# Performance work log

Hardware: AMD Instinct MI355X
Metric: run time of the kernel (lower is better)

The kernel has to match this reference:

```python
import jax, jax.numpy as jnp
import numpy as np

B_, T_, F_, N_ = 16, 12, 32, 500
L_, K_ = 3, 2
DIL = (1, 2, 4)


def setup_inputs() -> dict:
    key = jax.random.key(0)
    ks = jax.random.split(key, 12)
    f = jnp.float32
    return {
        "node_embeddings": jax.random.normal(ks[0], (B_, T_, F_, N_), f),
        "B_mat": jax.random.normal(ks[1], (F_, F_), f) * 0.1,
        "static_MTE": jax.random.normal(ks[2], (T_, N_, N_), f),
        "learnable_adj": jax.random.normal(ks[3], (T_, N_, N_), f),
        "conv_w": jax.random.normal(ks[4], (L_, F_, F_, 1, K_), f) * 0.1,
        "conv_b": jnp.zeros((L_, F_), f),
        "gcn_w": jax.random.normal(ks[5], (L_, F_, F_), f) * 0.1,
        "gcn_b": jnp.zeros((L_, F_), f),
        "gate_w": jax.random.normal(ks[6], (F_, F_), f) * 0.1,
        "gate_b": jnp.zeros((F_,), f),
        "att_Wa": jax.random.normal(ks[7], (F_, F_), f) * 0.1,
        "att_ba": jnp.zeros((F_,), f),
        "att_v": jax.random.normal(ks[8], (F_, 1), f) * 0.1,
        "use_MTE": 1,
        "batch_index": 2,
        "is_training": 1,
    }


def reference(node_embeddings, B_mat, static_MTE, learnable_adj, conv_w, conv_b,
              gcn_w, gcn_b, gate_w, gate_b, att_Wa, att_ba, att_v,
              use_MTE, batch_index, is_training):
    Bz, T, Fd, N = node_embeddings.shape
    L = conv_w.shape[0]

    # ---- dynamic adjacency: relu->softmax of U_{t-k} B U_t^T, for every k ----
    U = jnp.transpose(node_embeddings, (0, 1, 3, 2))        # [B,T,N,F]
    U_t = U[:, -1]                                          # [B,N,F]
    scores = jnp.einsum('btnf,fg,bmg->btnm', U, B_mat, U_t)  # [B,T,N,N]
    dyn = jax.nn.softmax(jax.nn.relu(scores), axis=-1)
    # batch_index != 1, training: learnable adjacency accumulated with dynamic one
    batch_dyn = learnable_adj[None] + dyn                   # module state update; GCNConv
    del batch_dyn                                           # drops edge weights, so Y does not depend on it

    # ---- dilated layers ----
    # GCNConv over dense_to_sparse(softmax adjacency): all N*N entries > 0, edge
    # weights are discarded -> propagation matrix P = (J + I) / (N + 1)
    x = node_embeddings                                     # [B,T,F,N]
    res_agg = []
    for li in range(L):
        residual = x
        X = jnp.transpose(x, (0, 1, 3, 2))                  # [B,T,N,F]
        propX = (jnp.sum(X, axis=2, keepdims=True) + X) / (N + 1)
        gcn = jnp.einsum('btnf,fg->btng', propX, gcn_w[li]) + gcn_b[li]
        # use_gnn & use_MTE & use_dynamic_adj -> sigmoid gating (dropout = eval identity)
        gcn = jax.nn.sigmoid(jnp.einsum('btnf,fg->btng', gcn, gate_w) + gate_b)
        # causal-padded dilated temporal conv over T
        pad = (K_ - 1) * DIL[li]
        xp = jnp.pad(gcn, ((0, 0), (pad, 0), (0, 0), (0, 0)))   # [B,T+pad,N,F]
        xp = jnp.transpose(xp, (0, 3, 2, 1))                    # [B,F,N,T+pad]
        out = jax.lax.conv_general_dilated(
            xp, conv_w[li], window_strides=(1, 1), padding='VALID',
            rhs_dilation=(1, DIL[li]),
            dimension_numbers=('NCHW', 'OIHW', 'NCHW'))
        out = jax.nn.relu(out + conv_b[li][None, :, None, None])  # [B,F,N,T]
        res_agg.append(out[:, :, :, -1])                          # [B,F,N]
        x = jnp.transpose(out, (0, 3, 1, 2)) + residual           # [B,T,F,N]

    # ---- multi-range attention over layer outputs ----
    res = jnp.stack(res_agg, axis=3)                        # [B,F,N,L]
    res = jnp.transpose(res, (0, 2, 1, 3))                  # [B,N,F,L]
    xp2 = jnp.transpose(res, (0, 3, 1, 2))                  # [B,L,N,F]
    s = jnp.tanh(xp2 @ att_Wa + att_ba) @ att_v             # [B,L,N,1]
    # faithful to original: flat (B,L,N) buffer reinterpreted as (B,N,L)
    s = s.reshape(Bz, N, L)
    a = jax.nn.softmax(s, axis=2)                           # [B,N,L]
    Y = jnp.einsum('bnm,bnfm->bnf', a, res)                 # [B,N,F]
    return Y
```

## Files before the change

### kernel.cpp

```cpp
#include <hip/hip_runtime.h>
#include <math.h>

#define B_ 16
#define T_ 12
#define F_ 32
#define N_ 500
#define L_ 3
#define K_ 2
#define INV_N1 (1.0f / 501.0f)

__device__ __forceinline__ float sigmoidf_(float x) {
    return 1.f / (1.f + __expf(-x));
}

__global__ __launch_bounds__(256) void prep_kernel(
        const float* __restrict__ x0,
        const float* __restrict__ gcn_w, const float* __restrict__ gcn_b,
        const float* __restrict__ gate_w, const float* __restrict__ gate_b,
        float* __restrict__ Wc, float* __restrict__ bc,
        float* __restrict__ cs0, float* __restrict__ cs1,
        float* __restrict__ cs2) {
    const int bt = blockIdx.x;
    const int tid = threadIdx.x;

    if (tid < F_) {
        cs1[bt * F_ + tid] = 0.f;
        cs2[bt * F_ + tid] = 0.f;
    }

    const int f = tid >> 3, j = tid & 7;
    const float4* row = (const float4*)(x0 + ((size_t)bt * F_ + f) * N_);
    float s = 0.f;
    for (int j4 = j; j4 < 125; j4 += 8) {
        float4 v = row[j4];
        s += v.x + v.y + v.z + v.w;
    }
    s += __shfl_xor(s, 1, 64);
    s += __shfl_xor(s, 2, 64);
    s += __shfl_xor(s, 4, 64);
    if (j == 0) cs0[bt * F_ + f] = s;

    if (bt < L_) {
        const int li = bt;
        for (int idx = tid; idx < F_ * F_; idx += 256) {
            int fi = idx >> 5, fo = idx & 31;
            float a = 0.f;
#pragma unroll
            for (int m = 0; m < F_; ++m)
                a += gcn_w[(li * F_ + fi) * F_ + m] * gate_w[m * F_ + fo];
            Wc[li * F_ * F_ + idx] = a * INV_N1;
        }
        if (tid < F_) {
            float a = gate_b[tid];
#pragma unroll
            for (int m = 0; m < F_; ++m)
                a += gcn_b[li * F_ + m] * gate_w[m * F_ + tid];
            bc[li * F_ + tid] = a;
        }
    }
}

__global__ __launch_bounds__(512) void gcn_kernel(
        const float* __restrict__ xin,
        const float* __restrict__ Wc, const float* __restrict__ bc,
        const float* __restrict__ cs, int li, float* __restrict__ g) {
    __shared__ __align__(16) float sx[F_][128];
    __shared__ __align__(16) float sWc[F_ * F_];
    __shared__ float sbase[F_];

    const int blk = blockIdx.x;
    const int bt = blk >> 2, c = blk & 3;
    const int nbase = c * 128;
    const int nb4 = (c == 3) ? 29 : 32;
    const int tid = threadIdx.x;

    for (int idx = tid; idx < F_ * nb4; idx += 512) {
        int f = idx / nb4, j4 = idx % nb4;
        float4 v = *(const float4*)(xin + ((size_t)bt * F_ + f) * N_ + nbase + 4 * j4);
        ((float4*)&sx[f][0])[j4] = v;
    }
    for (int idx = tid; idx < 256; idx += 512)
        ((float4*)sWc)[idx] = ((const float4*)(Wc + li * F_ * F_))[idx];
    if (tid < F_) {
        float a = bc[li * F_ + tid];
#pragma unroll
        for (int fi = 0; fi < F_; ++fi)
            a += cs[bt * F_ + fi] * Wc[li * F_ * F_ + fi * F_ + tid];
        sbase[tid] = a;
    }
    __syncthreads();

    const int n = tid & 127, q = tid >> 7;
    const int gn = nbase + n;
    if (gn < N_) {
        float acc[8];
#pragma unroll
        for (int jj = 0; jj < 8; ++jj) acc[jj] = sbase[q * 8 + jj];
#pragma unroll
        for (int fi = 0; fi < F_; ++fi) {
            float xv = sx[fi][n];
#pragma unroll
            for (int jj = 0; jj < 8; ++jj)
                acc[jj] += xv * sWc[fi * F_ + q * 8 + jj];
        }
#pragma unroll
        for (int jj = 0; jj < 8; ++jj)
            g[((size_t)bt * F_ + q * 8 + jj) * N_ + gn] = sigmoidf_(acc[jj]);
    }
}

__global__ __launch_bounds__(512) void conv_kernel(
        const float* __restrict__ g,
        const float* __restrict__ conv_w, const float* __restrict__ conv_b,
        int li, int dil,
        const float* xin, float* xout,
        float* __restrict__ resP, float* __restrict__ cs_next, int do_cs) {
    __shared__ __align__(16) float sgc[F_][128];
    __shared__ __align__(16) float sgp[F_][128];
    __shared__ __align__(16) float sW[F_ * F_ * K_];
    __shared__ float sB[F_];

    const int blk = blockIdx.x;
    const int bt = blk >> 2, c = blk & 3;
    const int t = bt % T_, b = bt / T_;
    const int nbase = c * 128;
    const int nb4 = (c == 3) ? 29 : 32;
    const int tid = threadIdx.x;

    ((float4*)sW)[tid] = ((const float4*)(conv_w + (size_t)li * F_ * F_ * K_))[tid];
    if (tid < F_) sB[tid] = conv_b[li * F_ + tid];

    for (int idx = tid; idx < F_ * nb4; idx += 512) {
        int f = idx / nb4, j4 = idx % nb4;
        ((float4*)&sgc[f][0])[j4] =
            *(const float4*)(g + ((size_t)bt * F_ + f) * N_ + nbase + 4 * j4);
    }
    if (t >= dil) {
        for (int idx = tid; idx < F_ * nb4; idx += 512) {
            int f = idx / nb4, j4 = idx % nb4;
            ((float4*)&sgp[f][0])[j4] =
                *(const float4*)(g + ((size_t)(bt - dil) * F_ + f) * N_ + nbase + 4 * j4);
        }
    } else {
        for (int idx = tid; idx < F_ * nb4; idx += 512) {
            int f = idx / nb4, j4 = idx % nb4;
            ((float4*)&sgp[f][0])[j4] = make_float4(0.f, 0.f, 0.f, 0.f);
        }
    }
    __syncthreads();

    const int n = tid & 127, q = tid >> 7;
    const int gn = nbase + n;
    const bool valid = (gn < N_);

    float acc[8], xov[8];
#pragma unroll
    for (int jj = 0; jj < 8; ++jj) { acc[jj] = sB[q * 8 + jj]; xov[jj] = 0.f; }

    if (valid) {
#pragma unroll
        for (int fi = 0; fi < F_; ++fi) {
            float gp = sgp[fi][n], gc = sgc[fi][n];
#pragma unroll
            for (int jj = 0; jj < 8; ++jj) {
                const int fo = q * 8 + jj;
                acc[jj] += gp * sW[(fo * F_ + fi) * K_ + 0]
                         + gc * sW[(fo * F_ + fi) * K_ + 1];
            }
        }
#pragma unroll
        for (int jj = 0; jj < 8; ++jj) {
            const int fo = q * 8 + jj;
            float o = fmaxf(acc[jj], 0.f);
            float rv = xin[((size_t)bt * F_ + fo) * N_ + gn];
            float xo = o + rv;
            xout[((size_t)bt * F_ + fo) * N_ + gn] = xo;
            acc[jj] = o;
            xov[jj] = xo;
        }
        if (t == T_ - 1) {
            float* rs = resP + ((size_t)(li * B_ + b) * N_ + gn) * F_ + q * 8;
#pragma unroll
            for (int jj = 0; jj < 8; ++jj) rs[jj] = acc[jj];
        }
    }

    if (do_cs) {
        const int lane = tid & 63;
#pragma unroll
        for (int jj = 0; jj < 8; ++jj) {
            float s = xov[jj];
#pragma unroll
            for (int off = 32; off >= 1; off >>= 1) s += __shfl_xor(s, off, 64);
            if (lane == 0) atomicAdd(&cs_next[bt * F_ + q * 8 + jj], s);
        }
    }
}

__global__ __launch_bounds__(192) void att_kernel(
        const float* __restrict__ resP,
        const float* __restrict__ Wa, const float* __restrict__ ba,
        const float* __restrict__ v, float* __restrict__ out) {
    __shared__ __align__(16) float sWa[F_ * F_];
    __shared__ float sScore[2][L_];
    const int tid = threadIdx.x;
    for (int idx = tid; idx < F_ * F_; idx += 192) sWa[idx] = Wa[idx];
    __syncthreads();

    const int pair = blockIdx.x;
    const int b = pair / 250;
    const int base_n = (pair % 250) * 2;
    const int gIdx = tid >> 5;
    const int fo = tid & 31;
    const int o = gIdx / 3, l = gIdx % 3;
    const int n = base_n + o;
    const int j = n * 3 + l;
    const int lp = j / N_, np = j % N_;

    const float vv = v[fo];
    const float* r = resP + ((size_t)(lp * B_ + b) * N_ + np) * F_;
    float acc = ba[fo];
#pragma unroll
    for (int f = 0; f < F_; ++f) acc += r[f] * sWa[f * F_ + fo];
    float s = tanhf(acc) * vv;
#pragma unroll
    for (int off = 16; off >= 1; off >>= 1) s += __shfl_xor(s, off, 64);
    if (fo == 0) sScore[o][l] = s;
    __syncthreads();

    if (tid < 64) {
        const int oo = tid >> 5, f = tid & 31;
        const int nn = base_n + oo;
        const float s0 = sScore[oo][0], s1 = sScore[oo][1], s2 = sScore[oo][2];
        const float m = fmaxf(fmaxf(s0, s1), s2);
        const float e0 = __expf(s0 - m), e1 = __expf(s1 - m), e2 = __expf(s2 - m);
        const float inv = 1.f / (e0 + e1 + e2);
        const float r0 = resP[((size_t)(0 * B_ + b) * N_ + nn) * F_ + f];
        const float r1 = resP[((size_t)(1 * B_ + b) * N_ + nn) * F_ + f];
        const float r2 = resP[((size_t)(2 * B_ + b) * N_ + nn) * F_ + f];
        out[(size_t)(b * N_ + nn) * F_ + f] = (e0 * r0 + e1 * r1 + e2 * r2) * inv;
    }
}

extern "C" void kernel_launch(void* const* d_in, const int* in_sizes, int n_in,
                              void* d_out, int out_size, void* d_ws, size_t ws_size,
                              hipStream_t stream) {
    const float* x0      = (const float*)d_in[0];
    const float* conv_w  = (const float*)d_in[4];
    const float* conv_b  = (const float*)d_in[5];
    const float* gcn_w   = (const float*)d_in[6];
    const float* gcn_b   = (const float*)d_in[7];
    const float* gate_w  = (const float*)d_in[8];
    const float* gate_b  = (const float*)d_in[9];
    const float* att_Wa  = (const float*)d_in[10];
    const float* att_ba  = (const float*)d_in[11];
    const float* att_v   = (const float*)d_in[12];

    float* ws = (float*)d_ws;
    float* x    = ws;
    float* g    = x + 3072000;
    float* resP = g + 3072000;
    float* Wc   = resP + 768000;
    float* bc   = Wc + 3072;
    float* cs0  = bc + 96;
    float* cs1  = cs0 + 6144;
    float* cs2  = cs1 + 6144;

    prep_kernel<<<B_ * T_, 256, 0, stream>>>(x0, gcn_w, gcn_b, gate_w, gate_b,
                                             Wc, bc, cs0, cs1, cs2);

    gcn_kernel<<<B_ * T_ * 4, 512, 0, stream>>>(x0, Wc, bc, cs0, 0, g);
    conv_kernel<<<B_ * T_ * 4, 512, 0, stream>>>(g, conv_w, conv_b, 0, 1,
                                                 x0, x, resP, cs1, 1);
    gcn_kernel<<<B_ * T_ * 4, 512, 0, stream>>>(x, Wc, bc, cs1, 1, g);
    conv_kernel<<<B_ * T_ * 4, 512, 0, stream>>>(g, conv_w, conv_b, 1, 2,
                                                 x, x, resP, cs2, 1);
    gcn_kernel<<<B_ * T_ * 4, 512, 0, stream>>>(x, Wc, bc, cs2, 2, g);
    conv_kernel<<<B_ * T_ * 4, 512, 0, stream>>>(g, conv_w, conv_b, 2, 4,
                                                 x, x, resP, cs0, 0);

    att_kernel<<<(B_ * N_) / 2, 192, 0, stream>>>(resP, att_Wa, att_ba, att_v,
                                                  (float*)d_out);
}
```

Before: 202.8 us.

## Fuse GCN gate and dilated conv into one per-layer kernel with recompute

Merges the gcn and conv kernels into a single layer kernel that computes the sigmoid gate for the current timestep and recomputes it for the dilated previous timestep from x, instead of writing and reading g through global memory. This removes three kernel launches and the g round trip, and reads the residual from shared memory. In exchange the gate matmul is done twice per block when a previous timestep exists, and x is ping-ponged between two buffers.

```diff
diff --git a/kernel.cpp b/kernel.cpp
--- a/kernel.cpp
+++ b/kernel.cpp
@@ -60,64 +60,17 @@
     }
 }
 
-__global__ __launch_bounds__(512) void gcn_kernel(
-        const float* __restrict__ xin,
+__global__ __launch_bounds__(512, 6) void layer_kernel(
+        const float* __restrict__ xin, float* __restrict__ xout,
+        const float* __restrict__ conv_w, const float* __restrict__ conv_b,
         const float* __restrict__ Wc, const float* __restrict__ bc,
-        const float* __restrict__ cs, int li, float* __restrict__ g) {
-    __shared__ __align__(16) float sx[F_][128];
+        const float* __restrict__ cs, int li, int dil,
+        float* __restrict__ resP, float* __restrict__ cs_next, int do_cs) {
+    __shared__ __align__(16) float A[F_][128];
+    __shared__ __align__(16) float Bt[F_][128];
+    __shared__ __align__(16) float sW[F_ * F_ * K_];
     __shared__ __align__(16) float sWc[F_ * F_];
-    __shared__ float sbase[F_];
-
-    const int blk = blockIdx.x;
-    const int bt = blk >> 2, c = blk & 3;
-    const int nbase = c * 128;
-    const int nb4 = (c == 3) ? 29 : 32;
-    const int tid = threadIdx.x;
-
-    for (int idx = tid; idx < F_ * nb4; idx += 512) {
-        int f = idx / nb4, j4 = idx % nb4;
-        float4 v = *(const float4*)(xin + ((size_t)bt * F_ + f) * N_ + nbase + 4 * j4);
-        ((float4*)&sx[f][0])[j4] = v;
-    }
-    for (int idx = tid; idx < 256; idx += 512)
-        ((float4*)sWc)[idx] = ((const float4*)(Wc + li * F_ * F_))[idx];
-    if (tid < F_) {
-        float a = bc[li * F_ + tid];
-#pragma unroll
-        for (int fi = 0; fi < F_; ++fi)
-            a += cs[bt * F_ + fi] * Wc[li * F_ * F_ + fi * F_ + tid];
-        sbase[tid] = a;
-    }
-    __syncthreads();
-
-    const int n = tid & 127, q = tid >> 7;
-    const int gn = nbase + n;
-    if (gn < N_) {
-        float acc[8];
-#pragma unroll
-        for (int jj = 0; jj < 8; ++jj) acc[jj] = sbase[q * 8 + jj];
-#pragma unroll
-        for (int fi = 0; fi < F_; ++fi) {
-            float xv = sx[fi][n];
-#pragma unroll
-            for (int jj = 0; jj < 8; ++jj)
-                acc[jj] += xv * sWc[fi * F_ + q * 8 + jj];
-        }
-#pragma unroll
-        for (int jj = 0; jj < 8; ++jj)
-            g[((size_t)bt * F_ + q * 8 + jj) * N_ + gn] = sigmoidf_(acc[jj]);
-    }
-}
-
-__global__ __launch_bounds__(512) void conv_kernel(
-        const float* __restrict__ g,
-        const float* __restrict__ conv_w, const float* __restrict__ conv_b,
-        int li, int dil,
-        const float* xin, float* xout,
-        float* __restrict__ resP, float* __restrict__ cs_next, int do_cs) {
-    __shared__ __align__(16) float sgc[F_][128];
-    __shared__ __align__(16) float sgp[F_][128];
-    __shared__ __align__(16) float sW[F_ * F_ * K_];
+    __shared__ float sbase[2][F_];
     __shared__ float sB[F_];
 
     const int blk = blockIdx.x;
@@ -126,60 +79,115 @@
     const int nbase = c * 128;
     const int nb4 = (c == 3) ? 29 : 32;
     const int tid = threadIdx.x;
+    const bool hasprev = (t >= dil);
 
     ((float4*)sW)[tid] = ((const float4*)(conv_w + (size_t)li * F_ * F_ * K_))[tid];
+    if (tid < 256)
+        ((float4*)sWc)[tid] = ((const float4*)(Wc + li * F_ * F_))[tid];
     if (tid < F_) sB[tid] = conv_b[li * F_ + tid];
-
+    if (tid >= 320 && tid < 320 + F_) {
+        const int fo = tid - 320;
+        const float* cw = Wc + li * F_ * F_;
+        float a = bc[li * F_ + fo];
+#pragma unroll
+        for (int fi = 0; fi < F_; ++fi) a += cs[bt * F_ + fi] * cw[fi * F_ + fo];
+        sbase[0][fo] = a;
+    }
+    if (hasprev && tid >= 384 && tid < 384 + F_) {
+        const int fo = tid - 384;
+        const float* cw = Wc + li * F_ * F_;
+        float a = bc[li * F_ + fo];
+#pragma unroll
+        for (int fi = 0; fi < F_; ++fi)
+            a += cs[(bt - dil) * F_ + fi] * cw[fi * F_ + fo];
+        sbase[1][fo] = a;
+    }
     for (int idx = tid; idx < F_ * nb4; idx += 512) {
         int f = idx / nb4, j4 = idx % nb4;
-        ((float4*)&sgc[f][0])[j4] =
-            *(const float4*)(g + ((size_t)bt * F_ + f) * N_ + nbase + 4 * j4);
-    }
-    if (t >= dil) {
-        for (int idx = tid; idx < F_ * nb4; idx += 512) {
-            int f = idx / nb4, j4 = idx % nb4;
-            ((float4*)&sgp[f][0])[j4] =
-                *(const float4*)(g + ((size_t)(bt - dil) * F_ + f) * N_ + nbase + 4 * j4);
-        }
-    } else {
-        for (int idx = tid; idx < F_ * nb4; idx += 512) {
-            int f = idx / nb4, j4 = idx % nb4;
-            ((float4*)&sgp[f][0])[j4] = make_float4(0.f, 0.f, 0.f, 0.f);
-        }
+        ((float4*)&A[f][0])[j4] =
+            *(const float4*)(xin + ((size_t)bt * F_ + f) * N_ + nbase + 4 * j4);
     }
     __syncthreads();
 
     const int n = tid & 127, q = tid >> 7;
     const int gn = nbase + n;
     const bool valid = (gn < N_);
-
-    float acc[8], xov[8];
-#pragma unroll
-    for (int jj = 0; jj < 8; ++jj) { acc[jj] = sB[q * 8 + jj]; xov[jj] = 0.f; }
-
+    const int fo0 = q * 8;
+
+    float rv[8], gc[8];
+#pragma unroll
+    for (int jj = 0; jj < 8; ++jj) {
+        rv[jj] = A[fo0 + jj][n];
+        gc[jj] = sbase[0][fo0 + jj];
+    }
+#pragma unroll
+    for (int fi = 0; fi < F_; ++fi) {
+        float xv = A[fi][n];
+#pragma unroll
+        for (int jj = 0; jj < 8; ++jj) gc[jj] += xv * sWc[fi * F_ + fo0 + jj];
+    }
+#pragma unroll
+    for (int jj = 0; jj < 8; ++jj) Bt[fo0 + jj][n] = sigmoidf_(gc[jj]);
+
+    if (hasprev) {
+        __syncthreads();
+        for (int idx = tid; idx < F_ * nb4; idx += 512) {
+            int f = idx / nb4, j4 = idx % nb4;
+            ((float4*)&A[f][0])[j4] = *(const float4*)(
+                xin + ((size_t)(bt - dil) * F_ + f) * N_ + nbase + 4 * j4);
+        }
+        __syncthreads();
+        float gp[8];
+#pragma unroll
+        for (int jj = 0; jj < 8; ++jj) gp[jj] = sbase[1][fo0 + jj];
+#pragma unroll
+        for (int fi = 0; fi < F_; ++fi) {
+            float xv = A[fi][n];
+#pragma unroll
+            for (int jj = 0; jj < 8; ++jj) gp[jj] += xv * sWc[fi * F_ + fo0 + jj];
+        }
+        __syncthreads();
+#pragma unroll
+        for (int jj = 0; jj < 8; ++jj) A[fo0 + jj][n] = sigmoidf_(gp[jj]);
+    }
+    __syncthreads();
+
+    float acc[8];
+#pragma unroll
+    for (int jj = 0; jj < 8; ++jj) acc[jj] = sB[fo0 + jj];
+    if (hasprev) {
+#pragma unroll
+        for (int fi = 0; fi < F_; ++fi) {
+            float gpv = A[fi][n], gcv = Bt[fi][n];
+#pragma unroll
+            for (int jj = 0; jj < 8; ++jj)
+                acc[jj] += gpv * sW[((fo0 + jj) * F_ + fi) * K_ + 0]
+                         + gcv * sW[((fo0 + jj) * F_ + fi) * K_ + 1];
+        }
+    } else {
+#pragma unroll
+        for (int fi = 0; fi < F_; ++fi) {
+            float gcv = Bt[fi][n];
+#pragma unroll
+            for (int jj = 0; jj < 8; ++jj)
+                acc[jj] += gcv * sW[((fo0 + jj) * F_ + fi) * K_ + 1];
+        }
+    }
+
+    float xov[8];
+#pragma unroll
+    for (int jj = 0; jj < 8; ++jj) xov[jj] = 0.f;
     if (valid) {
 #pragma unroll
-        for (int fi = 0; fi < F_; ++fi) {
-            float gp = sgp[fi][n], gc = sgc[fi][n];
-#pragma unroll
-            for (int jj = 0; jj < 8; ++jj) {
-                const int fo = q * 8 + jj;
-                acc[jj] += gp * sW[(fo * F_ + fi) * K_ + 0]
-                         + gc * sW[(fo * F_ + fi) * K_ + 1];
-            }
-        }
-#pragma unroll
         for (int jj = 0; jj < 8; ++jj) {
-            const int fo = q * 8 + jj;
             float o = fmaxf(acc[jj], 0.f);
-            float rv = xin[((size_t)bt * F_ + fo) * N_ + gn];
-            float xo = o + rv;
-            xout[((size_t)bt * F_ + fo) * N_ + gn] = xo;
+            float xo = o + rv[jj];
+            xout[((size_t)bt * F_ + fo0 + jj) * N_ + gn] = xo;
             acc[jj] = o;
             xov[jj] = xo;
         }
         if (t == T_ - 1) {
-            float* rs = resP + ((size_t)(li * B_ + b) * N_ + gn) * F_ + q * 8;
+            float* rs = resP + ((size_t)(li * B_ + b) * N_ + gn) * F_ + fo0;
 #pragma unroll
             for (int jj = 0; jj < 8; ++jj) rs[jj] = acc[jj];
         }
@@ -192,7 +200,7 @@
             float s = xov[jj];
 #pragma unroll
             for (int off = 32; off >= 1; off >>= 1) s += __shfl_xor(s, off, 64);
-            if (lane == 0) atomicAdd(&cs_next[bt * F_ + q * 8 + jj], s);
+            if (lane == 0) atomicAdd(&cs_next[bt * F_ + fo0 + jj], s);
         }
     }
 }
@@ -257,9 +265,9 @@
     const float* att_v   = (const float*)d_in[12];
 
     float* ws = (float*)d_ws;
-    float* x    = ws;
-    float* g    = x + 3072000;
-    float* resP = g + 3072000;
+    float* xA   = ws;
+    float* xB   = xA + 3072000;
+    float* resP = xB + 3072000;
     float* Wc   = resP + 768000;
     float* bc   = Wc + 3072;
     float* cs0  = bc + 96;
@@ -269,15 +277,15 @@
     prep_kernel<<<B_ * T_, 256, 0, stream>>>(x0, gcn_w, gcn_b, gate_w, gate_b,
                                              Wc, bc, cs0, cs1, cs2);
 
-    gcn_kernel<<<B_ * T_ * 4, 512, 0, stream>>>(x0, Wc, bc, cs0, 0, g);
-    conv_kernel<<<B_ * T_ * 4, 512, 0, stream>>>(g, conv_w, conv_b, 0, 1,
-                                                 x0, x, resP, cs1, 1);
-    gcn_kernel<<<B_ * T_ * 4, 512, 0, stream>>>(x, Wc, bc, cs1, 1, g);
-    conv_kernel<<<B_ * T_ * 4, 512, 0, stream>>>(g, conv_w, conv_b, 1, 2,
-                                                 x, x, resP, cs2, 1);
-    gcn_kernel<<<B_ * T_ * 4, 512, 0, stream>>>(x, Wc, bc, cs2, 2, g);
-    conv_kernel<<<B_ * T_ * 4, 512, 0, stream>>>(g, conv_w, conv_b, 2, 4,
-                                                 x, x, resP, cs0, 0);
+    layer_kernel<<<B_ * T_ * 4, 512, 0, stream>>>(x0, xA, conv_w, conv_b,
+                                                  Wc, bc, cs0, 0, 1,
+                                                  resP, cs1, 1);
+    layer_kernel<<<B_ * T_ * 4, 512, 0, stream>>>(xA, xB, conv_w, conv_b,
+                                                  Wc, bc, cs1, 1, 2,
+                                                  resP, cs2, 1);
+    layer_kernel<<<B_ * T_ * 4, 512, 0, stream>>>(xB, xA, conv_w, conv_b,
+                                                  Wc, bc, cs2, 2, 4,
+                                                  resP, cs1, 0);
 
     att_kernel<<<(B_ * N_) / 2, 192, 0, stream>>>(resP, att_Wa, att_ba, att_v,
                                                   (float*)d_out);
```

Measured after the change: 240.6 us. 18.6% more time.
